# Kernel tuning notes

Measured on AMD Instinct MI355X. Metric: run time of the kernel, lower is better.

The kernel has to match this reference:

```python
import jax, jax.numpy as jnp
import numpy as np

H, D = 8, 16
F = H * D              # hidden_dim = 128
L = 2                  # num HGT layers
NS = [50000, 20000, 10000]                     # gene, disease, drug node counts
EDGE_META = [(0, 0), (0, 1), (2, 0), (2, 1)]   # (src_type, dst_type) per edge type
ES = [300000, 150000, 100000, 50000]
OFFS = [0, NS[0], NS[0] + NS[1], NS[0] + NS[1] + NS[2]]
NTOT = OFFS[-1]
R, T = len(EDGE_META), len(NS)
SQRT_D = float(np.sqrt(D))


def setup_inputs() -> dict:
    key = jax.random.key(0)
    ks = jax.random.split(key, 32)
    inp = {}
    inp["x_gene"] = jax.random.normal(ks[0], (NS[0], F), jnp.float32)
    inp["x_disease"] = jax.random.normal(ks[1], (NS[1], F), jnp.float32)
    inp["x_drug"] = jax.random.normal(ks[2], (NS[2], F), jnp.float32)
    inp["Wkqv"] = 0.05 * jax.random.normal(ks[3], (L, T, F, 3 * F), jnp.float32)
    inp["bkqv"] = jnp.zeros((L, T, 3 * F), jnp.float32)
    inp["Ak"] = 0.1 * jax.random.normal(ks[4], (L, R, H, D, D), jnp.float32)
    inp["Av"] = 0.1 * jax.random.normal(ks[5], (L, R, H, D, D), jnp.float32)
    inp["prel"] = jnp.ones((L, R, H), jnp.float32)   # PyG inits p_rel to ones
    inp["Wout"] = 0.05 * jax.random.normal(ks[6], (L, T, F, F), jnp.float32)
    inp["bout"] = jnp.zeros((L, T, F), jnp.float32)
    inp["skip"] = jnp.ones((L, T), jnp.float32)      # PyG inits skip to 1
    names = ["ei_gg", "ei_gd", "ei_rg", "ei_rd"]
    for i, (name, (st, dt), E) in enumerate(zip(names, EDGE_META, ES)):
        src = jax.random.randint(ks[10 + 2 * i], (E,), 0, NS[st], dtype=jnp.int32)
        dst = jax.random.randint(ks[11 + 2 * i], (E,), 0, NS[dt], dtype=jnp.int32)
        inp[name] = jnp.stack([src, dst])
    return inp


def _hgt_layer(xs, eis, Wkqv_l, bkqv_l, Ak_l, Av_l, prel_l, Wout_l, bout_l, skip_l):
    """One PyG-style HGTConv layer over the heterogeneous graph."""
    kqv = [x @ Wkqv_l[t] + bkqv_l[t] for t, x in enumerate(xs)]
    k = [a[:, :F].reshape(-1, H, D) for a in kqv]
    q = [a[:, F:2 * F].reshape(-1, H, D) for a in kqv]
    v = [a[:, 2 * F:].reshape(-1, H, D) for a in kqv]

    alphas, dsts, ves = [], [], []
    for r, (st, dt) in enumerate(EDGE_META):
        src, dst = eis[r][0], eis[r][1]
        # relation-specific per-head transforms applied on source node set
        k_r = jnp.einsum('nhd,hde->nhe', k[st], Ak_l[r])
        v_r = jnp.einsum('nhd,hde->nhe', v[st], Av_l[r])
        ke = k_r[src]                      # [E, H, D]
        ve = v_r[src]                      # [E, H, D]
        qe = q[dt][dst]                    # [E, H, D]
        a = (qe * ke).sum(-1) * prel_l[r] / SQRT_D   # [E, H]
        alphas.append(a)
        dsts.append(dst + OFFS[dt])
        ves.append(ve)
    alpha = jnp.concatenate(alphas, 0)     # [Etot, H]
    dstg = jnp.concatenate(dsts, 0)        # [Etot]
    ve = jnp.concatenate(ves, 0)           # [Etot, H, D]

    # segment softmax over all incoming edges per destination node
    amax = jax.ops.segment_max(alpha, dstg, num_segments=NTOT)
    ex = jnp.exp(alpha - amax[dstg])
    denom = jax.ops.segment_sum(ex, dstg, num_segments=NTOT)
    w = ex / denom[dstg]
    out = jax.ops.segment_sum(ve * w[..., None], dstg, num_segments=NTOT)
    out = out.reshape(NTOT, F)

    new_xs = []
    for t, x in enumerate(xs):
        o_t = out[OFFS[t]:OFFS[t + 1]]
        o = jax.nn.gelu(o_t, approximate=False) @ Wout_l[t] + bout_l[t]
        a_s = jax.nn.sigmoid(skip_l[t])
        new_xs.append(a_s * o + (1.0 - a_s) * x)
    return new_xs


def reference(x_gene, x_disease, x_drug, Wkqv, bkqv, Ak, Av, prel, Wout, bout,
              skip, ei_gg, ei_gd, ei_rg, ei_rd):
    xs = [x_gene, x_disease, x_drug]
    eis = [ei_gg, ei_gd, ei_rg, ei_rd]
    for l in range(L):
        new = _hgt_layer(xs, eis, Wkqv[l], bkqv[l], Ak[l], Av[l], prel[l],
                         Wout[l], bout[l], skip[l])
        # encoder: dropout(relu(conv_out)) + residual; dropout = identity (eval)
        xs = [jax.nn.relu(n) + x for n, x in zip(new, xs)]
    return tuple(xs)
```

## Files before the change

kernel.cpp:

```cpp
#include <hip/hip_runtime.h>


#define NTOT  80000
#define ETOT  600000
#define NSRC  120000

typedef unsigned short u16;
typedef unsigned int   u32;
typedef __attribute__((ext_vector_type(8))) short short8;
typedef __attribute__((ext_vector_type(4))) float f32x4;

__device__ __forceinline__ float bf2f(u16 u){
  union { u32 i; float f; } v; v.i = ((u32)u) << 16; return v.f;
}
__device__ __forceinline__ u16 f2bf(float f){
  union { float f; u32 i; } v; v.f = f;
  u32 x = v.i;
  return (u16)((x + 0x7fffu + ((x >> 16) & 1u)) >> 16);
}
__device__ __forceinline__ void unp4(uint4 a, float* o){
  union { u32 i; float f; } t;
  t.i = a.x << 16;        o[0]=t.f;  t.i = a.x & 0xffff0000u; o[1]=t.f;
  t.i = a.y << 16;        o[2]=t.f;  t.i = a.y & 0xffff0000u; o[3]=t.f;
  t.i = a.z << 16;        o[4]=t.f;  t.i = a.z & 0xffff0000u; o[5]=t.f;
  t.i = a.w << 16;        o[6]=t.f;  t.i = a.w & 0xffff0000u; o[7]=t.f;
}
__device__ __forceinline__ void load16bf(const u16* p, float* o){
  unp4(*(const uint4*)p, o); unp4(*(const uint4*)(p + 8), o + 8);
}


__global__ __launch_bounds__(256) void copy_init(
    const float* __restrict__ xg, const float* __restrict__ xd,
    const float* __restrict__ xr, float* __restrict__ X, u16* __restrict__ Xbf)
{
  int i = blockIdx.x * 256 + threadIdx.x;
  if (i >= 2560000) return;
  const float* src; int off;
  if (i < 1600000)      { src = xg; off = i; }
  else if (i < 2240000) { src = xd; off = i - 1600000; }
  else                  { src = xr; off = i - 2240000; }
  float4 v = ((const float4*)src)[off];
  ((float4*)X)[i] = v;
  uint2 b;
  b.x = (u32)f2bf(v.x) | ((u32)f2bf(v.y) << 16);
  b.y = (u32)f2bf(v.z) | ((u32)f2bf(v.w) << 16);
  ((uint2*)Xbf)[i] = b;
}

__global__ __launch_bounds__(256) void zero_cc(int* __restrict__ cnt, int* __restrict__ cur){
  int i = blockIdx.x * 256 + threadIdx.x;
  if (i < NTOT){ cnt[i] = 0; cur[i] = 0; }
}


__global__ __launch_bounds__(256) void count_all(
    const int* __restrict__ e0, const int* __restrict__ e1,
    const int* __restrict__ e2, const int* __restrict__ e3,
    int* __restrict__ cnt)
{
  int e = blockIdx.x * 256 + threadIdx.x;
  if (e >= ETOT) return;
  const int* ei; int E, loc, offd;
  if (e < 300000)      { ei = e0; E = 300000; loc = e;          offd = 0; }
  else if (e < 450000) { ei = e1; E = 150000; loc = e - 300000; offd = 50000; }
  else if (e < 550000) { ei = e2; E = 100000; loc = e - 450000; offd = 0; }
  else                 { ei = e3; E = 50000;  loc = e - 550000; offd = 50000; }
  atomicAdd(&cnt[offd + ei[E + loc]], 1);
}

__global__ __launch_bounds__(256) void scan_partial(const int* __restrict__ cnt,
                             int* __restrict__ rowp, int* __restrict__ bsum){
  __shared__ int s[256];
  int tid = threadIdx.x;
  int i = blockIdx.x * 256 + tid;
  int v = (i < NTOT) ? cnt[i] : 0;
  s[tid] = v; __syncthreads();
  for (int off = 1; off < 256; off <<= 1){
    int t = (tid >= off) ? s[tid - off] : 0;
    __syncthreads();
    s[tid] += t;
    __syncthreads();
  }
  if (i < NTOT) rowp[i] = s[tid] - v;
  if (tid == 255) bsum[blockIdx.x] = s[255];
}

__global__ __launch_bounds__(256) void scan_block(int* __restrict__ bsum, int nb){
  __shared__ int b[512];
  __shared__ int p[256];
  int tid = threadIdx.x;
  b[tid]       = (tid < nb)       ? bsum[tid]       : 0;
  b[tid + 256] = (tid + 256 < nb) ? bsum[tid + 256] : 0;
  __syncthreads();
  int pv = b[2*tid] + b[2*tid + 1];
  p[tid] = pv; __syncthreads();
  for (int off = 1; off < 256; off <<= 1){
    int t = (tid >= off) ? p[tid - off] : 0;
    __syncthreads();
    p[tid] += t;
    __syncthreads();
  }
  int excl = p[tid] - pv;
  int e0 = excl, e1 = excl + b[2*tid];
  __syncthreads();
  if (2*tid < nb)   bsum[2*tid]     = e0;
  if (2*tid+1 < nb) bsum[2*tid + 1] = e1;
}

__global__ __launch_bounds__(256) void scan_add(int* __restrict__ rowp, const int* __restrict__ bsum){
  int i = blockIdx.x * 256 + threadIdx.x;
  if (i < NTOT) rowp[i] += bsum[i >> 8];
}

__global__ __launch_bounds__(256) void scatter_all(
    const int* __restrict__ e0, const int* __restrict__ e1,
    const int* __restrict__ e2, const int* __restrict__ e3,
    const int* __restrict__ rowp, int* __restrict__ cur,
    int* __restrict__ elist)
{
  int e = blockIdx.x * 256 + threadIdx.x;
  if (e >= ETOT) return;
  const int* ei; int E, loc, offd, rnoff, rel;
  if (e < 300000)      { ei = e0; E = 300000; loc = e;          offd = 0;     rnoff = 0;      rel = 0; }
  else if (e < 450000) { ei = e1; E = 150000; loc = e - 300000; offd = 50000; rnoff = 50000;  rel = 1; }
  else if (e < 550000) { ei = e2; E = 100000; loc = e - 450000; offd = 0;     rnoff = 100000; rel = 2; }
  else                 { ei = e3; E = 50000;  loc = e - 550000; offd = 50000; rnoff = 110000; rel = 3; }
  int src = ei[loc], dst = ei[E + loc];
  int dstg = offd + dst;
  int pos = atomicAdd(&cur[dstg], 1);
  elist[rowp[dstg] + pos] = ((rnoff + src) << 2) | rel;
}


__global__ __launch_bounds__(256) void build_weff(
    const float* __restrict__ Wkqv, const float* __restrict__ Ak,
    const float* __restrict__ Av, float* __restrict__ Weff)
{
  int lr = blockIdx.y;
  int l = lr >> 2, r = lr & 3;
  int st = (r >= 2) ? 2 : 0;
  int elem = blockIdx.x * 256 + threadIdx.x;
  int f = elem >> 8, j = elem & 255;
  const float* W = Wkqv + (size_t)(l*3 + st) * 49152;
  float acc = 0.f;
  if (j < 128){
    int h = j >> 4, e = j & 15;
    const float* Am = Ak + (size_t)(l*4 + r) * 2048 + h*256;
#pragma unroll
    for (int d = 0; d < 16; d++) acc += W[f*384 + h*16 + d] * Am[d*16 + e];
  } else {
    int j2 = j - 128, h = j2 >> 4, e = j2 & 15;
    const float* Am = Av + (size_t)(l*4 + r) * 2048 + h*256;
#pragma unroll
    for (int d = 0; d < 16; d++) acc += W[f*384 + 256 + h*16 + d] * Am[d*16 + e];
  }
  Weff[(size_t)lr * 32768 + elem] = acc;
}

__global__ __launch_bounds__(256) void build_beff(
    const float* __restrict__ bkqv, const float* __restrict__ Ak,
    const float* __restrict__ Av, float* __restrict__ beff)
{
  int lr = blockIdx.x;
  int l = lr >> 2, r = lr & 3;
  int st = (r >= 2) ? 2 : 0;
  int j = threadIdx.x;
  const float* b = bkqv + (size_t)(l*3 + st) * 384;
  float acc = 0.f;
  if (j < 128){
    int h = j >> 4, e = j & 15;
    const float* Am = Ak + (size_t)(l*4 + r) * 2048 + h*256;
#pragma unroll
    for (int d = 0; d < 16; d++) acc += b[h*16 + d] * Am[d*16 + e];
  } else {
    int j2 = j - 128, h = j2 >> 4, e = j2 & 15;
    const float* Am = Av + (size_t)(l*4 + r) * 2048 + h*256;
#pragma unroll
    for (int d = 0; d < 16; d++) acc += b[256 + h*16 + d] * Am[d*16 + e];
  }
  beff[lr * 256 + j] = acc;
}


__global__ __launch_bounds__(256) void conv_wq(const float* __restrict__ Wkqv, u16* __restrict__ WqT){
  int i = blockIdx.x * 256 + threadIdx.x;
  if (i >= 6*16384) return;
  int lt = i >> 14, rem = i & 16383, n = rem >> 7, k = rem & 127;
  WqT[i] = f2bf(Wkqv[(size_t)lt*49152 + k*384 + 128 + n]);
}

__global__ __launch_bounds__(256) void conv_weff(const float* __restrict__ Weff, u16* __restrict__ WeffT){
  int i = blockIdx.x * 256 + threadIdx.x;
  if (i >= 8*32768) return;
  int lr = i >> 15, rem = i & 32767, n = rem >> 7, k = rem & 127;
  WeffT[i] = f2bf(Weff[(size_t)lr*32768 + k*256 + n]);
}

__global__ __launch_bounds__(256) void conv_wout(const float* __restrict__ Wout, u16* __restrict__ WoutT){
  int i = blockIdx.x * 256 + threadIdx.x;
  if (i >= 6*16384) return;
  int lt = i >> 14, rem = i & 16383, n = rem >> 7, k = rem & 127;
  WoutT[i] = f2bf(Wout[(size_t)lt*16384 + k*128 + n]);
}


__device__ __forceinline__ void stage_bt(const u16* __restrict__ src, u16* BTl){
  int tid = threadIdx.x;
  const uint4* g = (const uint4*)src;
  uint4 tmp[8];
#pragma unroll
  for (int i = 0; i < 8; i++) tmp[i] = g[tid + i*256];
#pragma unroll
  for (int i = 0; i < 8; i++){
    int L = (tid + i*256) * 16;
    int Ls = L ^ (((L >> 8) & 7) << 4);
    *(uint4*)((char*)BTl + Ls) = tmp[i];
  }
  __syncthreads();
}

__device__ __forceinline__ void gemm_core(
    const u16* __restrict__ A, const u16* BTl, int M, int bm,
    f32x4 acc[8][2])
{
  int tid = threadIdx.x;
  int lane = tid & 63, w = tid >> 6;
  int quad = lane >> 4, lm = lane & 15;
  short8 af[2][4];
#pragma unroll
  for (int mf = 0; mf < 2; mf++){
    int row = bm + w*32 + mf*16 + lm;
    if (row < M){
      const u16* ap = A + (size_t)row*128 + quad*8;
#pragma unroll
      for (int c = 0; c < 4; c++) af[mf][c] = *(const short8*)(ap + c*32);
    } else {
      short8 z = {0,0,0,0,0,0,0,0};
#pragma unroll
      for (int c = 0; c < 4; c++) af[mf][c] = z;
    }
  }
#pragma unroll
  for (int nt = 0; nt < 8; nt++)
#pragma unroll
    for (int mf = 0; mf < 2; mf++) acc[nt][mf] = (f32x4){0.f,0.f,0.f,0.f};
#pragma unroll
  for (int nt = 0; nt < 8; nt++){
    int rowb = nt*16 + lm;
    int base = rowb*256 + quad*16;
    int sw = (rowb & 7) << 4;
#pragma unroll
    for (int c = 0; c < 4; c++){
      short8 bf = *(const short8*)((const char*)BTl + ((base + c*64) ^ sw));
      acc[nt][0] = __builtin_amdgcn_mfma_f32_16x16x32_bf16(af[0][c], bf, acc[nt][0], 0, 0, 0);
      acc[nt][1] = __builtin_amdgcn_mfma_f32_16x16x32_bf16(af[1][c], bf, acc[nt][1], 0, 0, 0);
    }
  }
}

__global__ __launch_bounds__(256) void mfma_gemm_q(
    const u16* __restrict__ Xbf, const u16* __restrict__ WqTl,
    const float* __restrict__ bl, u16* __restrict__ qg)
{
  __shared__ u16 BTl[16384];
  int by = blockIdx.x;
  int t, bm, M, roff;
  if (by < 391)      { t = 0; bm = by*128;        M = 50000; roff = 0; }
  else if (by < 548) { t = 1; bm = (by-391)*128;  M = 20000; roff = 50000; }
  else               { t = 2; bm = (by-548)*128;  M = 10000; roff = 70000; }
  stage_bt(WqTl + (size_t)t*16384, BTl);
  const u16* A = Xbf + (size_t)roff*128;
  const float* bias = bl + (size_t)t*384 + 128;
  u16* C = qg + (size_t)roff*128;
  f32x4 acc[8][2];
  gemm_core(A, BTl, M, bm, acc);
  int lane = threadIdx.x & 63, w = threadIdx.x >> 6;
  int quad = lane >> 4, lm = lane & 15;
#pragma unroll
  for (int nt = 0; nt < 8; nt++){
    int col = nt*16 + lm;
    float bb = bias[col];
#pragma unroll
    for (int mf = 0; mf < 2; mf++)
#pragma unroll
      for (int i = 0; i < 4; i++){
        int r = bm + w*32 + mf*16 + quad*4 + i;
        if (r < M) C[(size_t)r*128 + col] = f2bf(acc[nt][mf][i] + bb);
      }
  }
}

__global__ __launch_bounds__(256) void mfma_gemm_kv(
    const u16* __restrict__ Xbf, const u16* __restrict__ WeffTl,
    const float* __restrict__ beffl, u16* __restrict__ kv)
{
  __shared__ u16 BTl[16384];
  int by = blockIdx.y;
  int r, bm, M, soff, ooff;
  if (by < 391)      { r = 0; bm = by*128;        M = 50000; soff = 0;     ooff = 0; }
  else if (by < 782) { r = 1; bm = (by-391)*128;  M = 50000; soff = 0;     ooff = 50000; }
  else if (by < 861) { r = 2; bm = (by-782)*128;  M = 10000; soff = 70000; ooff = 100000; }
  else               { r = 3; bm = (by-861)*128;  M = 10000; soff = 70000; ooff = 110000; }
  int bn = blockIdx.x * 128;
  stage_bt(WeffTl + (size_t)r*32768 + (size_t)bn*128, BTl);
  const u16* A = Xbf + (size_t)soff*128;
  const float* bias = beffl + (size_t)r*256;
  u16* C = kv + (size_t)ooff*256;
  f32x4 acc[8][2];
  gemm_core(A, BTl, M, bm, acc);
  int lane = threadIdx.x & 63, w = threadIdx.x >> 6;
  int quad = lane >> 4, lm = lane & 15;
#pragma unroll
  for (int nt = 0; nt < 8; nt++){
    int col = bn + nt*16 + lm;
    float bb = bias[col];
#pragma unroll
    for (int mf = 0; mf < 2; mf++)
#pragma unroll
      for (int i = 0; i < 4; i++){
        int r2 = bm + w*32 + mf*16 + quad*4 + i;
        if (r2 < M) C[(size_t)r2*256 + col] = f2bf(acc[nt][mf][i] + bb);
      }
  }
}

__global__ __launch_bounds__(256) void mfma_gemm_out(
    const u16* __restrict__ Gall, const u16* __restrict__ WoutTl,
    const float* __restrict__ bl, const float* __restrict__ skipl,
    float* __restrict__ Xall, u16* __restrict__ Xbfall)
{
  __shared__ u16 BTl[16384];
  int by = blockIdx.x;
  int t, bm, M, roff;
  if (by < 391)      { t = 0; bm = by*128;        M = 50000; roff = 0; }
  else if (by < 548) { t = 1; bm = (by-391)*128;  M = 20000; roff = 50000; }
  else               { t = 2; bm = (by-548)*128;  M = 10000; roff = 70000; }
  stage_bt(WoutTl + (size_t)t*16384, BTl);
  const u16* A = Gall + (size_t)roff*128;
  const float* bias = bl + (size_t)t*128;
  float* X = Xall + (size_t)roff*128;
  u16* Xb = Xbfall + (size_t)roff*128;
  f32x4 acc[8][2];
  gemm_core(A, BTl, M, bm, acc);
  float a_s = 1.f / (1.f + expf(-skipl[t]));
  float b_s = 1.f - a_s;
  int lane = threadIdx.x & 63, w = threadIdx.x >> 6;
  int quad = lane >> 4, lm = lane & 15;
#pragma unroll
  for (int nt = 0; nt < 8; nt++){
    int col = nt*16 + lm;
    float bb = bias[col];
#pragma unroll
    for (int mf = 0; mf < 2; mf++)
#pragma unroll
      for (int i = 0; i < 4; i++){
        int r = bm + w*32 + mf*16 + quad*4 + i;
        if (r < M){
          float* xp = X + (size_t)r*128 + col;
          float x = *xp;
          float o = acc[nt][mf][i] + bb;
          float xn = fmaxf(a_s*o + b_s*x, 0.f) + x;
          *xp = xn;
          Xb[(size_t)r*128 + col] = f2bf(xn);
        }
      }
  }
}


__global__ __launch_bounds__(256) void attn_kernel(
    u16* __restrict__ qg,
    const u16* __restrict__ kv,
    const float* __restrict__ prel,
    const int* __restrict__ rowp, const int* __restrict__ cnt,
    const int* __restrict__ elist)
{
  int gid = blockIdx.x * 256 + threadIdx.x;
  int n = gid >> 3, h = gid & 7;
  if (n >= NTOT) return;
  float sc0 = prel[0*8+h]*0.25f, sc1 = prel[1*8+h]*0.25f,
        sc2 = prel[2*8+h]*0.25f, sc3 = prel[3*8+h]*0.25f;
  float q[16];
  load16bf(qg + (size_t)n * 128 + h*16, q);
  float acc[16] = {};
  float dsum = 0.f;
  int start = rowp[n], c = cnt[n];

  auto edge = [&](int ev, uint4 ka, uint4 kb, uint4 va, uint4 vb){
    float ke[16], ve[16];
    unp4(ka, ke); unp4(kb, ke + 8);
    unp4(va, ve); unp4(vb, ve + 8);
    float a = 0.f;
#pragma unroll
    for (int d = 0; d < 16; d++) a += q[d] * ke[d];
    int r = ev & 3;
    float s = (r == 0) ? sc0 : (r == 1) ? sc1 : (r == 2) ? sc2 : sc3;
    float ex = expf(a * s);
    dsum += ex;
#pragma unroll
    for (int d = 0; d < 16; d++) acc[d] += ex * ve[d];
  };

  int ii = 0;
#pragma unroll 1
  for (; ii + 4 <= c; ii += 4){
    int e0 = elist[start + ii + 0], e1 = elist[start + ii + 1],
        e2 = elist[start + ii + 2], e3 = elist[start + ii + 3];
    const u16* p0 = kv + (size_t)(e0 >> 2) * 256 + h*16;
    const u16* p1 = kv + (size_t)(e1 >> 2) * 256 + h*16;
    const u16* p2 = kv + (size_t)(e2 >> 2) * 256 + h*16;
    const u16* p3 = kv + (size_t)(e3 >> 2) * 256 + h*16;
    uint4 k0a = *(const uint4*)p0,         k0b = *(const uint4*)(p0 + 8);
    uint4 k1a = *(const uint4*)p1,         k1b = *(const uint4*)(p1 + 8);
    uint4 k2a = *(const uint4*)p2,         k2b = *(const uint4*)(p2 + 8);
    uint4 k3a = *(const uint4*)p3,         k3b = *(const uint4*)(p3 + 8);
    uint4 v0a = *(const uint4*)(p0 + 128), v0b = *(const uint4*)(p0 + 136);
    uint4 v1a = *(const uint4*)(p1 + 128), v1b = *(const uint4*)(p1 + 136);
    uint4 v2a = *(const uint4*)(p2 + 128), v2b = *(const uint4*)(p2 + 136);
    uint4 v3a = *(const uint4*)(p3 + 128), v3b = *(const uint4*)(p3 + 136);
    edge(e0, k0a, k0b, v0a, v0b);
    edge(e1, k1a, k1b, v1a, v1b);
    edge(e2, k2a, k2b, v2a, v2b);
    edge(e3, k3a, k3b, v3a, v3b);
  }
  for (; ii < c; ii++){
    int ev = elist[start + ii];
    const u16* p = kv + (size_t)(ev >> 2) * 256 + h*16;
    uint4 ka = *(const uint4*)p,         kb = *(const uint4*)(p + 8);
    uint4 va = *(const uint4*)(p + 128), vb = *(const uint4*)(p + 136);
    edge(ev, ka, kb, va, vb);
  }

  float inv = (c > 0) ? 1.f / dsum : 0.f;
  u16 o[16];
#pragma unroll
  for (int d = 0; d < 16; d++){
    float x = acc[d] * inv;
    o[d] = f2bf(0.5f * x * (1.f + erff(x * 0.70710678118654752f)));
  }
  uint4 p0, p1;
  p0.x = o[0]|(o[1]<<16);   p0.y = o[2]|(o[3]<<16);
  p0.z = o[4]|(o[5]<<16);   p0.w = o[6]|(o[7]<<16);
  p1.x = o[8]|(o[9]<<16);   p1.y = o[10]|(o[11]<<16);
  p1.z = o[12]|(o[13]<<16); p1.w = o[14]|(o[15]<<16);
  u16* op = qg + (size_t)n * 128 + h*16;
  *(uint4*)op = p0; *(uint4*)(op + 8) = p1;
}


extern "C" void kernel_launch(void* const* d_in, const int* in_sizes, int n_in,
                              void* d_out, int out_size, void* d_ws, size_t ws_size,
                              hipStream_t stream)
{
  const float* xg   = (const float*)d_in[0];
  const float* xd   = (const float*)d_in[1];
  const float* xr_  = (const float*)d_in[2];
  const float* Wkqv = (const float*)d_in[3];
  const float* bkqv = (const float*)d_in[4];
  const float* Ak   = (const float*)d_in[5];
  const float* Av   = (const float*)d_in[6];
  const float* prel = (const float*)d_in[7];
  const float* Wout = (const float*)d_in[8];
  const float* bout = (const float*)d_in[9];
  const float* skip = (const float*)d_in[10];
  const int* ei[4] = {(const int*)d_in[11], (const int*)d_in[12],
                      (const int*)d_in[13], (const int*)d_in[14]};

  float* X = (float*)d_out;

  char* p = (char*)d_ws;
  auto alloc = [&](size_t b)->void*{ void* r = (void*)p; p += (b + 255) & ~(size_t)255; return r; };
  int*   cnt   = (int*)  alloc((size_t)NTOT * 4);
  int*   rowp  = (int*)  alloc((size_t)NTOT * 4);
  int*   cur   = (int*)  alloc((size_t)NTOT * 4);
  int*   bsum  = (int*)  alloc(512 * 4);
  int*   elist = (int*)  alloc((size_t)ETOT * 4);
  float* Weff  = (float*)alloc((size_t)8 * 32768 * 4);
  float* beff  = (float*)alloc((size_t)8 * 256 * 4);
  u16*   qg    = (u16*)  alloc((size_t)NTOT * 128 * 2);
  u16*   kv    = (u16*)  alloc((size_t)NSRC * 256 * 2);
  u16*   Xbf   = (u16*)  alloc((size_t)NTOT * 128 * 2);
  u16*   WqT   = (u16*)  alloc((size_t)6 * 16384 * 2);
  u16*   WeffT = (u16*)  alloc((size_t)8 * 32768 * 2);
  u16*   WoutT = (u16*)  alloc((size_t)6 * 16384 * 2);
  (void)ws_size; (void)in_sizes; (void)n_in; (void)out_size;

  copy_init<<<10000, 256, 0, stream>>>(xg, xd, xr_, X, Xbf);
  zero_cc<<<313, 256, 0, stream>>>(cnt, cur);

  count_all<<<(ETOT+255)/256, 256, 0, stream>>>(ei[0], ei[1], ei[2], ei[3], cnt);
  scan_partial<<<313, 256, 0, stream>>>(cnt, rowp, bsum);
  scan_block<<<1, 256, 0, stream>>>(bsum, 313);
  scan_add<<<313, 256, 0, stream>>>(rowp, bsum);
  scatter_all<<<(ETOT+255)/256, 256, 0, stream>>>(ei[0], ei[1], ei[2], ei[3], rowp, cur, elist);

  build_weff<<<dim3(128, 8), 256, 0, stream>>>(Wkqv, Ak, Av, Weff);
  build_beff<<<8, 256, 0, stream>>>(bkqv, Ak, Av, beff);
  conv_wq<<<384, 256, 0, stream>>>(Wkqv, WqT);
  conv_weff<<<1024, 256, 0, stream>>>(Weff, WeffT);
  conv_wout<<<384, 256, 0, stream>>>(Wout, WoutT);

  for (int l = 0; l < 2; l++){
    mfma_gemm_q<<<627, 256, 0, stream>>>(
        Xbf, WqT + (size_t)l*3*16384, bkqv + (size_t)l*3*384, qg);
    mfma_gemm_kv<<<dim3(2, 940), 256, 0, stream>>>(
        Xbf, WeffT + (size_t)l*4*32768, beff + (size_t)l*4*256, kv);
    attn_kernel<<<2500, 256, 0, stream>>>(qg, kv, prel + l*32, rowp, cnt, elist);
    mfma_gemm_out<<<627, 256, 0, stream>>>(
        qg, WoutT + (size_t)l*3*16384, bout + (size_t)l*3*128, skip + l*3, X, Xbf);
  }
}
```

Baseline: 470.1 us.

## Split attention edges across two thread halves and fuse weight prep kernels

```diff
diff --git a/kernel.cpp b/kernel.cpp
--- a/kernel.cpp
+++ b/kernel.cpp
@@ -133,29 +133,29 @@
 }
 
 
-__global__ __launch_bounds__(256) void build_weff(
+__global__ __launch_bounds__(256) void build_wefft(
     const float* __restrict__ Wkqv, const float* __restrict__ Ak,
-    const float* __restrict__ Av, float* __restrict__ Weff)
-{
-  int lr = blockIdx.y;
+    const float* __restrict__ Av, u16* __restrict__ WeffT)
+{
+  int i = blockIdx.x * 256 + threadIdx.x;
+  if (i >= 8*32768) return;
+  int lr = i >> 15, rem = i & 32767, n = rem >> 7, k = rem & 127;
   int l = lr >> 2, r = lr & 3;
   int st = (r >= 2) ? 2 : 0;
-  int elem = blockIdx.x * 256 + threadIdx.x;
-  int f = elem >> 8, j = elem & 255;
   const float* W = Wkqv + (size_t)(l*3 + st) * 49152;
   float acc = 0.f;
-  if (j < 128){
-    int h = j >> 4, e = j & 15;
+  if (n < 128){
+    int h = n >> 4, e = n & 15;
     const float* Am = Ak + (size_t)(l*4 + r) * 2048 + h*256;
 #pragma unroll
-    for (int d = 0; d < 16; d++) acc += W[f*384 + h*16 + d] * Am[d*16 + e];
+    for (int d = 0; d < 16; d++) acc += W[k*384 + h*16 + d] * Am[d*16 + e];
   } else {
-    int j2 = j - 128, h = j2 >> 4, e = j2 & 15;
+    int n2 = n - 128, h = n2 >> 4, e = n2 & 15;
     const float* Am = Av + (size_t)(l*4 + r) * 2048 + h*256;
 #pragma unroll
-    for (int d = 0; d < 16; d++) acc += W[f*384 + 256 + h*16 + d] * Am[d*16 + e];
-  }
-  Weff[(size_t)lr * 32768 + elem] = acc;
+    for (int d = 0; d < 16; d++) acc += W[k*384 + 256 + h*16 + d] * Am[d*16 + e];
+  }
+  WeffT[i] = f2bf(acc);
 }
 
 __global__ __launch_bounds__(256) void build_beff(
@@ -183,25 +183,20 @@
 }
 
 
-__global__ __launch_bounds__(256) void conv_wq(const float* __restrict__ Wkqv, u16* __restrict__ WqT){
+__global__ __launch_bounds__(256) void conv_w(
+    const float* __restrict__ Wkqv, const float* __restrict__ Wout,
+    u16* __restrict__ WqT, u16* __restrict__ WoutT)
+{
   int i = blockIdx.x * 256 + threadIdx.x;
-  if (i >= 6*16384) return;
-  int lt = i >> 14, rem = i & 16383, n = rem >> 7, k = rem & 127;
-  WqT[i] = f2bf(Wkqv[(size_t)lt*49152 + k*384 + 128 + n]);
-}
-
-__global__ __launch_bounds__(256) void conv_weff(const float* __restrict__ Weff, u16* __restrict__ WeffT){
-  int i = blockIdx.x * 256 + threadIdx.x;
-  if (i >= 8*32768) return;
-  int lr = i >> 15, rem = i & 32767, n = rem >> 7, k = rem & 127;
-  WeffT[i] = f2bf(Weff[(size_t)lr*32768 + k*256 + n]);
-}
-
-__global__ __launch_bounds__(256) void conv_wout(const float* __restrict__ Wout, u16* __restrict__ WoutT){
-  int i = blockIdx.x * 256 + threadIdx.x;
-  if (i >= 6*16384) return;
-  int lt = i >> 14, rem = i & 16383, n = rem >> 7, k = rem & 127;
-  WoutT[i] = f2bf(Wout[(size_t)lt*16384 + k*128 + n]);
+  if (i >= 2*6*16384) return;
+  if (i < 6*16384){
+    int lt = i >> 14, rem = i & 16383, n = rem >> 7, k = rem & 127;
+    WqT[i] = f2bf(Wkqv[(size_t)lt*49152 + k*384 + 128 + n]);
+  } else {
+    int j = i - 6*16384;
+    int lt = j >> 14, rem = j & 16383, n = rem >> 7, k = rem & 127;
+    WoutT[j] = f2bf(Wout[(size_t)lt*16384 + k*128 + n]);
+  }
 }
 
 
@@ -377,8 +372,11 @@
     const int* __restrict__ elist)
 {
   int gid = blockIdx.x * 256 + threadIdx.x;
-  int n = gid >> 3, h = gid & 7;
+  int n = gid >> 4;
   if (n >= NTOT) return;
+  int lane = threadIdx.x & 63;
+  int sub = (lane >> 3) & 1;
+  int h = lane & 7;
   float sc0 = prel[0*8+h]*0.25f, sc1 = prel[1*8+h]*0.25f,
         sc2 = prel[2*8+h]*0.25f, sc3 = prel[3*8+h]*0.25f;
   float q[16];
@@ -402,11 +400,11 @@
     for (int d = 0; d < 16; d++) acc[d] += ex * ve[d];
   };
 
-  int ii = 0;
+  int idx = sub;
 #pragma unroll 1
-  for (; ii + 4 <= c; ii += 4){
-    int e0 = elist[start + ii + 0], e1 = elist[start + ii + 1],
-        e2 = elist[start + ii + 2], e3 = elist[start + ii + 3];
+  for (; idx + 6 < c; idx += 8){
+    int e0 = elist[start + idx + 0], e1 = elist[start + idx + 2],
+        e2 = elist[start + idx + 4], e3 = elist[start + idx + 6];
     const u16* p0 = kv + (size_t)(e0 >> 2) * 256 + h*16;
     const u16* p1 = kv + (size_t)(e1 >> 2) * 256 + h*16;
     const u16* p2 = kv + (size_t)(e2 >> 2) * 256 + h*16;
@@ -424,28 +422,35 @@
     edge(e2, k2a, k2b, v2a, v2b);
     edge(e3, k3a, k3b, v3a, v3b);
   }
-  for (; ii < c; ii++){
-    int ev = elist[start + ii];
+#pragma unroll 1
+  for (; idx < c; idx += 2){
+    int ev = elist[start + idx];
     const u16* p = kv + (size_t)(ev >> 2) * 256 + h*16;
     uint4 ka = *(const uint4*)p,         kb = *(const uint4*)(p + 8);
     uint4 va = *(const uint4*)(p + 128), vb = *(const uint4*)(p + 136);
     edge(ev, ka, kb, va, vb);
   }
 
-  float inv = (c > 0) ? 1.f / dsum : 0.f;
-  u16 o[16];
-#pragma unroll
-  for (int d = 0; d < 16; d++){
-    float x = acc[d] * inv;
-    o[d] = f2bf(0.5f * x * (1.f + erff(x * 0.70710678118654752f)));
-  }
-  uint4 p0, p1;
-  p0.x = o[0]|(o[1]<<16);   p0.y = o[2]|(o[3]<<16);
-  p0.z = o[4]|(o[5]<<16);   p0.w = o[6]|(o[7]<<16);
-  p1.x = o[8]|(o[9]<<16);   p1.y = o[10]|(o[11]<<16);
-  p1.z = o[12]|(o[13]<<16); p1.w = o[14]|(o[15]<<16);
-  u16* op = qg + (size_t)n * 128 + h*16;
-  *(uint4*)op = p0; *(uint4*)(op + 8) = p1;
+  dsum += __shfl_xor(dsum, 8);
+#pragma unroll
+  for (int d = 0; d < 16; d++) acc[d] += __shfl_xor(acc[d], 8);
+
+  if (sub == 0){
+    float inv = (c > 0) ? 1.f / dsum : 0.f;
+    u16 o[16];
+#pragma unroll
+    for (int d = 0; d < 16; d++){
+      float x = acc[d] * inv;
+      o[d] = f2bf(0.5f * x * (1.f + erff(x * 0.70710678118654752f)));
+    }
+    uint4 p0, p1;
+    p0.x = o[0]|(o[1]<<16);   p0.y = o[2]|(o[3]<<16);
+    p0.z = o[4]|(o[5]<<16);   p0.w = o[6]|(o[7]<<16);
+    p1.x = o[8]|(o[9]<<16);   p1.y = o[10]|(o[11]<<16);
+    p1.z = o[12]|(o[13]<<16); p1.w = o[14]|(o[15]<<16);
+    u16* op = qg + (size_t)n * 128 + h*16;
+    *(uint4*)op = p0; *(uint4*)(op + 8) = p1;
+  }
 }
 
 
@@ -476,7 +481,6 @@
   int*   cur   = (int*)  alloc((size_t)NTOT * 4);
   int*   bsum  = (int*)  alloc(512 * 4);
   int*   elist = (int*)  alloc((size_t)ETOT * 4);
-  float* Weff  = (float*)alloc((size_t)8 * 32768 * 4);
   float* beff  = (float*)alloc((size_t)8 * 256 * 4);
   u16*   qg    = (u16*)  alloc((size_t)NTOT * 128 * 2);
   u16*   kv    = (u16*)  alloc((size_t)NSRC * 256 * 2);
@@ -495,18 +499,16 @@
   scan_add<<<313, 256, 0, stream>>>(rowp, bsum);
   scatter_all<<<(ETOT+255)/256, 256, 0, stream>>>(ei[0], ei[1], ei[2], ei[3], rowp, cur, elist);
 
-  build_weff<<<dim3(128, 8), 256, 0, stream>>>(Wkqv, Ak, Av, Weff);
+  build_wefft<<<1024, 256, 0, stream>>>(Wkqv, Ak, Av, WeffT);
   build_beff<<<8, 256, 0, stream>>>(bkqv, Ak, Av, beff);
-  conv_wq<<<384, 256, 0, stream>>>(Wkqv, WqT);
-  conv_weff<<<1024, 256, 0, stream>>>(Weff, WeffT);
-  conv_wout<<<384, 256, 0, stream>>>(Wout, WoutT);
+  conv_w<<<768, 256, 0, stream>>>(Wkqv, Wout, WqT, WoutT);
 
   for (int l = 0; l < 2; l++){
     mfma_gemm_q<<<627, 256, 0, stream>>>(
         Xbf, WqT + (size_t)l*3*16384, bkqv + (size_t)l*3*384, qg);
     mfma_gemm_kv<<<dim3(2, 940), 256, 0, stream>>>(
         Xbf, WeffT + (size_t)l*4*32768, beff + (size_t)l*4*256, kv);
-    attn_kernel<<<2500, 256, 0, stream>>>(qg, kv, prel + l*32, rowp, cnt, elist);
+    attn_kernel<<<5000, 256, 0, stream>>>(qg, kv, prel + l*32, rowp, cnt, elist);
     mfma_gemm_out<<<627, 256, 0, stream>>>(
         qg, WoutT + (size_t)l*3*16384, bout + (size_t)l*3*128, skip + l*3, X, Xbf);
   }
```

Measured after the change: 467.8 us. Within noise of the previous version (-0.5%).
